# Kernel optimization log

Hardware: AMD Instinct MI355X
Metric: run time of the kernel (lower is better)

Reference implementation:

```python
import jax, jax.numpy as jnp
import numpy as np
from jax import lax

DN = ('NCHW', 'OIHW', 'NCHW')


def conv_s2(x, w, b):
    # Conv2d(kernel=4, stride=2, padding=1): halves H,W
    y = lax.conv_general_dilated(x, w, (2, 2), ((1, 1), (1, 1)), dimension_numbers=DN)
    return y + b[None, :, None, None]


def conv_1x1(x, w, b):
    y = lax.conv_general_dilated(x, w, (1, 1), ((0, 0), (0, 0)), dimension_numbers=DN)
    return y + b[None, :, None, None]


def convT_s2(x, w, b):
    # torch ConvTranspose2d(kernel=4, stride=2, padding=1); torch weight layout [I,O,kh,kw]
    wt = jnp.flip(w, (2, 3)).transpose(1, 0, 2, 3)  # -> [O,I,kh,kw], spatially flipped
    y = lax.conv_general_dilated(x, wt, (1, 1), ((2, 2), (2, 2)),
                                 lhs_dilation=(2, 2), dimension_numbers=DN)
    return y + b[None, :, None, None]


def setup_inputs() -> dict:
    key = jax.random.key(0)
    ks = jax.random.split(key, 20)
    f32 = jnp.float32
    s = 0.05  # small init scale to keep activations sane
    inp = {
        'x': jax.random.uniform(ks[0], (32, 3, 256, 256), dtype=f32),
        # encoder
        'ew1': jax.random.normal(ks[1], (128, 3, 4, 4), f32) * s,
        'eb1': jnp.zeros((128,), f32),
        'ew2': jax.random.normal(ks[2], (256, 128, 4, 4), f32) * s,
        'eb2': jnp.zeros((256,), f32),
        'ew3': jax.random.normal(ks[3], (512, 256, 4, 4), f32) * s,
        'eb3': jnp.zeros((512,), f32),
        # pre-VQ 1x1 conv
        'pw': jax.random.normal(ks[4], (64, 512, 1, 1), f32) * s,
        'pb': jnp.zeros((64,), f32),
        # codebook (torch.randn in module)
        'emb': jax.random.normal(ks[5], (512, 64), f32),
        # decoder (ConvTranspose2d weights: [in, out, kh, kw])
        'dw1': jax.random.normal(ks[6], (64, 256, 4, 4), f32) * s,
        'db1': jnp.zeros((256,), f32),
        'dw2': jax.random.normal(ks[7], (256, 128, 4, 4), f32) * s,
        'db2': jnp.zeros((128,), f32),
        'dw3': jax.random.normal(ks[8], (128, 3, 4, 4), f32) * s,
        'db3': jnp.zeros((3,), f32),
    }
    return inp


def reference(x, ew1, eb1, ew2, eb2, ew3, eb3, pw, pb, emb,
              dw1, db1, dw2, db2, dw3, db3):
    # encoder
    h = jax.nn.relu(conv_s2(x, ew1, eb1))
    h = jax.nn.relu(conv_s2(h, ew2, eb2))
    h = jax.nn.relu(conv_s2(h, ew3, eb3))
    z_e = conv_1x1(h, pw, pb)  # [B, D, H, W]

    b, d, hh, ww = z_e.shape
    x_flat = z_e.reshape(b, d, hh * ww).transpose(0, 2, 1)  # [B, HW, D]
    # squared distances via expansion (same math, no [B,HW,K,D] blowup)
    x2 = jnp.sum(x_flat ** 2, axis=-1, keepdims=True)        # [B, HW, 1]
    e2 = jnp.sum(emb ** 2, axis=-1)                          # [K]
    dist = x2 - 2.0 * jnp.einsum('bnd,kd->bnk', x_flat, emb) + e2[None, None, :]
    indices = jnp.argmin(dist, axis=2)                       # [B, HW]
    zq_flat = emb[indices]                                   # [B, HW, D]
    z_q = zq_flat.transpose(0, 2, 1).reshape(b, d, hh, ww)

    quant_loss = (jnp.mean((zq_flat - x_flat) ** 2) * 2.0)   # matches detach-symmetric mse in fwd value

    # decoder
    y = jax.nn.relu(convT_s2(z_q, dw1, db1))
    y = jax.nn.relu(convT_s2(y, dw2, db2))
    y = jax.nn.sigmoid(convT_s2(y, dw3, db3))
    return (y, quant_loss)
```

## Files before the change

### kernel.cpp

```cpp
#include <hip/hip_runtime.h>
#include <cstddef>

typedef __attribute__((ext_vector_type(8))) _Float16 half8;
typedef __attribute__((ext_vector_type(4))) float f32x4;


template<int CIN>
__global__ __launch_bounds__(256) void wsplit_k(
    const float* __restrict__ W, _Float16* __restrict__ Wh,
    _Float16* __restrict__ Wl, int Cout) {
  constexpr int NCB = CIN / 32;
  int idx = blockIdx.x * 256 + threadIdx.x;
  if (idx >= Cout * CIN) return;
  int ci = idx % CIN, co = idx / CIN;
  int cb = ci >> 5, k8 = (ci >> 3) & 3, j = ci & 7;
  const float* wp = W + (size_t)idx * 16;
#pragma unroll
  for (int tap = 0; tap < 16; ++tap) {
    float w = wp[tap];
    _Float16 wh = (_Float16)w;
    _Float16 wl = (_Float16)((w - (float)wh) * 2048.0f);
    size_t o = (((size_t)(tap * NCB + cb) * 4 + k8) * Cout + co) * 8 + j;
    Wh[o] = wh; Wl[o] = wl;
  }
}

template<int CIN>
__global__ __launch_bounds__(256) void wsplitT_k(
    const float* __restrict__ W, _Float16* __restrict__ Wh,
    _Float16* __restrict__ Wl, int Cout) {
  constexpr int NCB = CIN / 32;
  int idx = blockIdx.x * 256 + threadIdx.x;
  if (idx >= CIN * Cout) return;
  int co = idx % Cout, ci = idx / Cout;
  int cb = ci >> 5, k8 = (ci >> 3) & 3, j = ci & 7;
  const float* wp = W + (size_t)idx * 16;
#pragma unroll
  for (int t = 0; t < 16; ++t) {
    int py = (t >> 3) & 1, px = (t >> 2) & 1, i0 = (t >> 1) & 1, i1 = t & 1;
    int kh = py ? (i0 ? 2 : 0) : (i0 ? 3 : 1);
    int kw = px ? (i1 ? 2 : 0) : (i1 ? 3 : 1);
    float w = wp[kh * 4 + kw];
    _Float16 wh = (_Float16)w;
    _Float16 wl = (_Float16)((w - (float)wh) * 2048.0f);
    size_t o = (((size_t)(t * NCB + cb) * 4 + k8) * Cout + co) * 8 + j;
    Wh[o] = wh; Wl[o] = wl;
  }
}

template<int CIN, int COUT, int CGRP, int RELU>
__global__ __launch_bounds__(256) void conv_mfma2(
    const float* __restrict__ in, const _Float16* __restrict__ Whg,
    const _Float16* __restrict__ Wlg, const float* __restrict__ bias,
    float* __restrict__ out, int Hin, int Win) {
  constexpr int NCB = CIN / 32;
  constexpr int MT  = COUT / CGRP;
  constexpr int MF  = MT / 64;
  const int Hout = Hin >> 1, Wout = Win >> 1;
  const int TW = Wout >> 4;
  __shared__ half8 Bh[4 * 346], Bl[4 * 346];
  const int tid = threadIdx.x;
  const int lane = tid & 63, w = tid >> 6;
  const int l15 = lane & 15, k8 = lane >> 4;
  const int tx = blockIdx.x % TW, ty = blockIdx.x / TW;
  const int cg = blockIdx.y % CGRP;
  const int b  = blockIdx.y / CGRP;
  const int oy0 = ty << 2, ox0 = tx << 4;
  const int iy_org = 2 * oy0 - 1, ix_org = 2 * ox0 - 1;
  const int cbase = cg * MT + w * (MT / 4);
  const float* ip = in + (size_t)b * CIN * Hin * Win;
  const size_t tapStride = (size_t)NCB * 4 * COUT * 8;
  const size_t HW = (size_t)Hin * Win;

  f32x4 accM[MF][4], accX[MF][4];
#pragma unroll
  for (int m = 0; m < MF; ++m)
#pragma unroll
    for (int nf = 0; nf < 4; ++nf) {
      accM[m][nf] = f32x4{0,0,0,0};
      accX[m][nf] = f32x4{0,0,0,0};
    }

  for (int cb = 0; cb < NCB; ++cb) {
    __syncthreads();
    for (int s = tid; s < 340; s += 256) {
      int hy = s / 34, hx = s - hy * 34;
      int iy = iy_org + hy, ix = ix_org + hx;
      bool ok = (unsigned)iy < (unsigned)Hin && (unsigned)ix < (unsigned)Win;
      const float* gp = ip + (size_t)cb * 32 * HW + (ptrdiff_t)iy * Win + ix;
      int slotBase = (hy * 2 + (hx & 1)) * 17 + (hx >> 1);
#pragma unroll
      for (int kk = 0; kk < 4; ++kk) {
        half8 vh, vl;
#pragma unroll
        for (int j = 0; j < 8; ++j) {
          float x = ok ? gp[(size_t)(kk * 8 + j) * HW] : 0.0f;
          _Float16 xh = (_Float16)x;
          vh[j] = xh; vl[j] = (_Float16)((x - (float)xh) * 2048.0f);
        }
        Bh[kk * 346 + slotBase] = vh;
        Bl[kk * 346 + slotBase] = vl;
      }
    }
    __syncthreads();
    const _Float16* aph = Whg + (((size_t)cb * 4 + k8) * COUT + cbase + l15) * 8;
    const _Float16* apl = Wlg + (((size_t)cb * 4 + k8) * COUT + cbase + l15) * 8;
    half8 ah[2][MF], al[2][MF];
#pragma unroll
    for (int m = 0; m < MF; ++m) {
      ah[0][m] = *(const half8*)(aph + m * 128);
      al[0][m] = *(const half8*)(apl + m * 128);
    }
#pragma unroll
    for (int tp = 0; tp < 16; ++tp) {
      const int cur = tp & 1, nxt = cur ^ 1;
      if (tp < 15) {
#pragma unroll
        for (int m = 0; m < MF; ++m) {
          ah[nxt][m] = *(const half8*)(aph + (size_t)(tp + 1) * tapStride + m * 128);
          al[nxt][m] = *(const half8*)(apl + (size_t)(tp + 1) * tapStride + m * 128);
        }
      }
      const int kh = tp >> 2, kw = tp & 3;
      const int p = kw & 1, cidx = kw >> 1;
#pragma unroll
      for (int nf = 0; nf < 4; ++nf) {
        const int slot = k8 * 346 + ((2 * nf + kh) * 2 + p) * 17 + l15 + cidx;
        const half8 bh = Bh[slot], bl = Bl[slot];
#pragma unroll
        for (int m = 0; m < MF; ++m) {
          accM[m][nf] = __builtin_amdgcn_mfma_f32_16x16x32_f16(ah[cur][m], bh, accM[m][nf], 0, 0, 0);
          accX[m][nf] = __builtin_amdgcn_mfma_f32_16x16x32_f16(ah[cur][m], bl, accX[m][nf], 0, 0, 0);
          accX[m][nf] = __builtin_amdgcn_mfma_f32_16x16x32_f16(al[cur][m], bh, accX[m][nf], 0, 0, 0);
        }
      }
    }
  }
#pragma unroll
  for (int m = 0; m < MF; ++m)
#pragma unroll
    for (int nf = 0; nf < 4; ++nf) {
      int oy = oy0 + nf, ox = ox0 + l15;
#pragma unroll
      for (int i = 0; i < 4; ++i) {
        int co = cbase + m * 16 + k8 * 4 + i;
        float v = accM[m][nf][i] + accX[m][nf][i] * (1.0f / 2048.0f) + bias[co];
        if (RELU) v = fmaxf(v, 0.0f);
        out[(((size_t)b * COUT + co) * Hout + oy) * Wout + ox] = v;
      }
    }
}

template<int CIN, int RELU>
__global__ __launch_bounds__(256) void convT_mfma(
    const float* __restrict__ in, const _Float16* __restrict__ Whg,
    const _Float16* __restrict__ Wlg, const float* __restrict__ bias,
    float* __restrict__ out, int Cout, int Hin, int Win) {
  constexpr int NCB = CIN / 32;
  const int Hout = Hin * 2, Wout = Win * 2;
  const int TW = Win >> 4;
  __shared__ half8 Bh[4 * 72], Bl[4 * 72];
  const int tid = threadIdx.x;
  const int lane = tid & 63, w = tid >> 6;
  const int l15 = lane & 15, k8 = lane >> 4;
  const int tx = blockIdx.x % TW, ty = blockIdx.x / TW;
  const int cbo = blockIdx.y % (Cout >> 6);
  const int b   = blockIdx.y / (Cout >> 6);
  const int ty0 = ty << 1, tx0 = tx << 4;
  const int co0 = (cbo << 6) + (w << 4);
  const float* ip = in + (size_t)b * CIN * Hin * Win;
  const size_t HW = (size_t)Hin * Win;
  const size_t tapStride = (size_t)NCB * 4 * Cout * 8;

  f32x4 accM[4][2], accX[4][2];
#pragma unroll
  for (int p = 0; p < 4; ++p)
#pragma unroll
    for (int nf = 0; nf < 2; ++nf) {
      accM[p][nf] = f32x4{0,0,0,0};
      accX[p][nf] = f32x4{0,0,0,0};
    }

  for (int cb = 0; cb < NCB; ++cb) {
    __syncthreads();
    for (int u = tid; u < 288; u += 256) {
      int pos = u % 72, kk = u / 72;
      int r = pos / 18, c = pos - r * 18;
      int iy = ty0 - 1 + r, ix = tx0 - 1 + c;
      bool ok = (unsigned)iy < (unsigned)Hin && (unsigned)ix < (unsigned)Win;
      const float* gp = ip + ((size_t)cb * 32 + kk * 8) * HW + (ptrdiff_t)iy * Win + ix;
      half8 vh, vl;
#pragma unroll
      for (int j = 0; j < 8; ++j) {
        float x = ok ? gp[(size_t)j * HW] : 0.0f;
        _Float16 xh = (_Float16)x;
        vh[j] = xh; vl[j] = (_Float16)((x - (float)xh) * 2048.0f);
      }
      Bh[kk * 72 + pos] = vh;
      Bl[kk * 72 + pos] = vl;
    }
    __syncthreads();
    const _Float16* aph = Whg + (((size_t)cb * 4 + k8) * Cout + co0 + l15) * 8;
    const _Float16* apl = Wlg + (((size_t)cb * 4 + k8) * Cout + co0 + l15) * 8;
    half8 ahA = *(const half8*)(aph);
    half8 alA = *(const half8*)(apl);
#pragma unroll
    for (int t = 0; t < 16; ++t) {
      half8 ahN, alN;
      if (t < 15) {
        ahN = *(const half8*)(aph + (size_t)(t + 1) * tapStride);
        alN = *(const half8*)(apl + (size_t)(t + 1) * tapStride);
      }
      const int py = (t >> 3) & 1, px = (t >> 2) & 1;
      const int i0 = (t >> 1) & 1, i1 = t & 1;
      const int dy = py ? (i0 ? 0 : 1) : (i0 ? -1 : 0);
      const int dx = px ? (i1 ? 0 : 1) : (i1 ? -1 : 0);
      const int p = py * 2 + px;
#pragma unroll
      for (int nf = 0; nf < 2; ++nf) {
        int slot = k8 * 72 + (nf + 1 + dy) * 18 + (l15 + 1 + dx);
        half8 bh = Bh[slot], bl = Bl[slot];
        accM[p][nf] = __builtin_amdgcn_mfma_f32_16x16x32_f16(ahA, bh, accM[p][nf], 0, 0, 0);
        accX[p][nf] = __builtin_amdgcn_mfma_f32_16x16x32_f16(ahA, bl, accX[p][nf], 0, 0, 0);
        accX[p][nf] = __builtin_amdgcn_mfma_f32_16x16x32_f16(alA, bh, accX[p][nf], 0, 0, 0);
      }
      if (t < 15) { ahA = ahN; alA = alN; }
    }
  }
#pragma unroll
  for (int nf = 0; nf < 2; ++nf) {
#pragma unroll
    for (int i = 0; i < 4; ++i) {
      int co = co0 + k8 * 4 + i;
      float bb = bias[co];
#pragma unroll
      for (int py = 0; py < 2; ++py) {
        float v0 = accM[py * 2 + 0][nf][i] + accX[py * 2 + 0][nf][i] * (1.0f / 2048.0f) + bb;
        float v1 = accM[py * 2 + 1][nf][i] + accX[py * 2 + 1][nf][i] * (1.0f / 2048.0f) + bb;
        if (RELU) { v0 = fmaxf(v0, 0.0f); v1 = fmaxf(v1, 0.0f); }
        int oy = 2 * (ty0 + nf) + py, ox = 2 * (tx0 + l15);
        *(float2*)(out + (((size_t)b * Cout + co) * Hout + oy) * Wout + ox) =
            make_float2(v0, v1);
      }
    }
  }
}


template<int CIN, int G, int RELU>
__global__ __launch_bounds__(256) void conv_t(
    const float* __restrict__ in, const float* __restrict__ wt,
    const float* __restrict__ bias, float* __restrict__ out,
    int Cout, int Hin, int Win) {
  const int Hout = Hin >> 1, Wout = Win >> 1;
  const int TW = Wout >> 4;
  __shared__ float tile[34 * 35];
  int tid = threadIdx.x;
  int oxl = tid & 15, oyl = tid >> 4;
  int tyt = blockIdx.x / TW, txt = blockIdx.x - tyt * TW;
  int oy0 = tyt << 4, ox0 = txt << 4;
  int cg = blockIdx.y % (Cout / G);
  int b  = blockIdx.y / (Cout / G);
  int co0 = cg * G;
  const int iy_org = 2 * oy0 - 1, ix_org = 2 * ox0 - 1;
  const float* ip = in + (size_t)b * CIN * Hin * Win;
  float acc[G];
#pragma unroll
  for (int j = 0; j < G; ++j) acc[j] = bias[co0 + j];
  const int lbase = (2 * oyl) * 35 + 2 * oxl;
  for (int ci = 0; ci < CIN; ++ci) {
    const float* ic = ip + (size_t)ci * Hin * Win;
    __syncthreads();
#pragma unroll
    for (int k = 0; k < 5; ++k) {
      int idx = tid + k * 256;
      if (idx < 34 * 34) {
        int r = idx / 34, c = idx - r * 34;
        int iy = iy_org + r, ix = ix_org + c;
        float v = ((unsigned)iy < (unsigned)Hin && (unsigned)ix < (unsigned)Win)
                      ? ic[(size_t)iy * Win + ix] : 0.0f;
        tile[r * 35 + c] = v;
      }
    }
    __syncthreads();
    float xv[16];
#pragma unroll
    for (int kh = 0; kh < 4; ++kh)
#pragma unroll
      for (int kw = 0; kw < 4; ++kw)
        xv[kh * 4 + kw] = tile[lbase + kh * 35 + kw];
    const float* wc = wt + ((size_t)co0 * CIN + ci) * 16;
#pragma unroll
    for (int j = 0; j < G; ++j) {
      const float* wj = wc + (size_t)j * CIN * 16;
#pragma unroll
      for (int t2 = 0; t2 < 16; ++t2) acc[j] = fmaf(xv[t2], wj[t2], acc[j]);
    }
  }
  size_t cs = (size_t)Hout * Wout;
  float* op = out + ((size_t)(b * Cout + co0) * Hout + (oy0 + oyl)) * Wout + ox0 + oxl;
#pragma unroll
  for (int j = 0; j < G; ++j) {
    float v = acc[j];
    if (RELU) v = fmaxf(v, 0.0f);
    op[(size_t)j * cs] = v;
  }
}

template<int CIN, int G>
__global__ __launch_bounds__(256) void conv1x1_k(
    const float* __restrict__ in, const float* __restrict__ wt,
    const float* __restrict__ bias, float* __restrict__ out,
    int Cout, int HW) {
  int hw = blockIdx.x * 256 + threadIdx.x;
  int cg = blockIdx.y % (Cout / G);
  int b  = blockIdx.y / (Cout / G);
  int co0 = cg * G;
  const float* ip = in + (size_t)b * CIN * HW + hw;
  float acc[G];
#pragma unroll
  for (int j = 0; j < G; ++j) acc[j] = bias[co0 + j];
#pragma unroll 4
  for (int ci = 0; ci < CIN; ++ci) {
    float xv = ip[(size_t)ci * HW];
#pragma unroll
    for (int j = 0; j < G; ++j)
      acc[j] = fmaf(xv, wt[(size_t)(co0 + j) * CIN + ci], acc[j]);
  }
  float* op = out + ((size_t)(b * Cout + co0)) * HW + hw;
#pragma unroll
  for (int j = 0; j < G; ++j) op[(size_t)j * HW] = acc[j];
}

__global__ __launch_bounds__(128) void vq_k(
    const float* __restrict__ ze, const float* __restrict__ emb,
    float* __restrict__ zq, float* __restrict__ partial) {
  __shared__ float4 se4[128 * 16];
  __shared__ float red[128];
  int tid = threadIdx.x;
  int gid = blockIdx.x * 128 + tid;
  int b = gid >> 10, n = gid & 1023;
  const float* zp = ze + ((size_t)b << 16) + n;
  float4 v4[16];
#pragma unroll
  for (int d = 0; d < 16; ++d) {
    v4[d].x = zp[(size_t)(4 * d + 0) << 10];
    v4[d].y = zp[(size_t)(4 * d + 1) << 10];
    v4[d].z = zp[(size_t)(4 * d + 2) << 10];
    v4[d].w = zp[(size_t)(4 * d + 3) << 10];
  }
  float best = 1e30f; int bi = 0;
  for (int c = 0; c < 4; ++c) {
    __syncthreads();
    for (int i = tid; i < 2048; i += 128)
      se4[i] = ((const float4*)emb)[(c << 11) + i];
    __syncthreads();
    for (int k = 0; k < 128; ++k) {
      const float4* e = se4 + (k << 4);
      float s = 0.0f;
#pragma unroll
      for (int d = 0; d < 16; ++d) {
        float4 ev = e[d];
        float t0 = v4[d].x - ev.x; s = fmaf(t0, t0, s);
        float t1 = v4[d].y - ev.y; s = fmaf(t1, t1, s);
        float t2 = v4[d].z - ev.z; s = fmaf(t2, t2, s);
        float t3 = v4[d].w - ev.w; s = fmaf(t3, t3, s);
      }
      if (s < best) { best = s; bi = (c << 7) + k; }
    }
  }
  const float4* eb4 = (const float4*)emb + ((size_t)bi << 4);
  float* qp = zq + ((size_t)b << 16) + n;
  float ls = 0.0f;
#pragma unroll
  for (int d = 0; d < 16; ++d) {
    float4 q = eb4[d];
    qp[(size_t)(4 * d + 0) << 10] = q.x;
    qp[(size_t)(4 * d + 1) << 10] = q.y;
    qp[(size_t)(4 * d + 2) << 10] = q.z;
    qp[(size_t)(4 * d + 3) << 10] = q.w;
    float t0 = q.x - v4[d].x; ls = fmaf(t0, t0, ls);
    float t1 = q.y - v4[d].y; ls = fmaf(t1, t1, ls);
    float t2 = q.z - v4[d].z; ls = fmaf(t2, t2, ls);
    float t3 = q.w - v4[d].w; ls = fmaf(t3, t3, ls);
  }
  red[tid] = ls;
  __syncthreads();
  for (int s = 64; s > 0; s >>= 1) {
    if (tid < s) red[tid] += red[tid + s];
    __syncthreads();
  }
  if (tid == 0) partial[blockIdx.x] = red[0];
}

__global__ __launch_bounds__(256) void loss_fin(
    const float* __restrict__ partial, float* __restrict__ out) {
  __shared__ float red[256];
  int t = threadIdx.x;
  red[t] = partial[t];
  __syncthreads();
  for (int s = 128; s > 0; s >>= 1) {
    if (t < s) red[t] += red[t + s];
    __syncthreads();
  }
  if (t == 0) out[0] = red[0] * (2.0f / 2097152.0f);
}

template<int CIN, int G, int ACT>
__global__ __launch_bounds__(256) void convT_t(
    const float* __restrict__ in, const float* __restrict__ wt,
    const float* __restrict__ bias, float* __restrict__ out,
    int Cout, int Hin, int Win) {
  const int Hout = Hin * 2, Wout = Win * 2;
  const int TW = Win >> 4;
  __shared__ float tile[18 * 19];
  int tid = threadIdx.x;
  int txl = tid & 15, tyl = tid >> 4;
  int tyt = blockIdx.x / TW, txt = blockIdx.x - tyt * TW;
  int ty0 = tyt << 4, tx0 = txt << 4;
  int og = blockIdx.y % (Cout / G);
  int b  = blockIdx.y / (Cout / G);
  int o0 = og * G;
  const int iy_org = ty0 - 1, ix_org = tx0 - 1;
  const float* ip = in + (size_t)b * CIN * Hin * Win;
  float a00[G], a01[G], a10[G], a11[G];
#pragma unroll
  for (int j = 0; j < G; ++j) {
    float bb = bias[o0 + j];
    a00[j] = bb; a01[j] = bb; a10[j] = bb; a11[j] = bb;
  }
  const int lb = tyl * 19 + txl;
  for (int i = 0; i < CIN; ++i) {
    const float* ic = ip + (size_t)i * Hin * Win;
    __syncthreads();
#pragma unroll
    for (int k = 0; k < 2; ++k) {
      int idx = tid + k * 256;
      if (idx < 18 * 18) {
        int r = idx / 18, c = idx - r * 18;
        int iy = iy_org + r, ix = ix_org + c;
        float v = ((unsigned)iy < (unsigned)Hin && (unsigned)ix < (unsigned)Win)
                      ? ic[(size_t)iy * Win + ix] : 0.0f;
        tile[r * 19 + c] = v;
      }
    }
    __syncthreads();
    float x00 = tile[lb],          x01 = tile[lb + 1],      x02 = tile[lb + 2];
    float x10 = tile[lb + 19],     x11 = tile[lb + 20],     x12 = tile[lb + 21];
    float x20 = tile[lb + 38],     x21 = tile[lb + 39],     x22 = tile[lb + 40];
    const float* wv = wt + ((size_t)i * Cout + o0) * 16;
#pragma unroll
    for (int j = 0; j < G; ++j) {
      const float* w4 = wv + j * 16;
      a00[j] = fmaf(x11, w4[5],  fmaf(x10, w4[7],  fmaf(x01, w4[13], fmaf(x00, w4[15], a00[j]))));
      a01[j] = fmaf(x12, w4[4],  fmaf(x11, w4[6],  fmaf(x02, w4[12], fmaf(x01, w4[14], a01[j]))));
      a10[j] = fmaf(x21, w4[1],  fmaf(x20, w4[3],  fmaf(x11, w4[9],  fmaf(x10, w4[11], a10[j]))));
      a11[j] = fmaf(x22, w4[0],  fmaf(x21, w4[2],  fmaf(x12, w4[8],  fmaf(x11, w4[10], a11[j]))));
    }
  }
  size_t cs = (size_t)Hout * Wout;
  int ty = ty0 + tyl, tx = tx0 + txl;
  size_t base = ((size_t)(b * Cout + o0) * Hout + 2 * (size_t)ty) * Wout + 2 * tx;
#pragma unroll
  for (int j = 0; j < G; ++j) {
    float v00 = a00[j], v01 = a01[j], v10 = a10[j], v11 = a11[j];
    if (ACT == 1) {
      v00 = fmaxf(v00, 0.0f); v01 = fmaxf(v01, 0.0f);
      v10 = fmaxf(v10, 0.0f); v11 = fmaxf(v11, 0.0f);
    } else if (ACT == 2) {
      v00 = 1.0f / (1.0f + expf(-v00)); v01 = 1.0f / (1.0f + expf(-v01));
      v10 = 1.0f / (1.0f + expf(-v10)); v11 = 1.0f / (1.0f + expf(-v11));
    }
    *(float2*)(out + base + (size_t)j * cs)        = make_float2(v00, v01);
    *(float2*)(out + base + (size_t)j * cs + Wout) = make_float2(v10, v11);
  }
}

extern "C" void kernel_launch(void* const* d_in, const int* in_sizes, int n_in,
                              void* d_out, int out_size, void* d_ws, size_t ws_size,
                              hipStream_t stream) {
  const float* x   = (const float*)d_in[0];
  const float* ew1 = (const float*)d_in[1];
  const float* eb1 = (const float*)d_in[2];
  const float* ew2 = (const float*)d_in[3];
  const float* eb2 = (const float*)d_in[4];
  const float* ew3 = (const float*)d_in[5];
  const float* eb3 = (const float*)d_in[6];
  const float* pw  = (const float*)d_in[7];
  const float* pb  = (const float*)d_in[8];
  const float* emb = (const float*)d_in[9];
  const float* dw1 = (const float*)d_in[10];
  const float* db1 = (const float*)d_in[11];
  const float* dw2 = (const float*)d_in[12];
  const float* db2 = (const float*)d_in[13];
  const float* dw3 = (const float*)d_in[14];
  const float* db3 = (const float*)d_in[15];
  float* out = (float*)d_out;
  char* ws = (char*)d_ws;

  const size_t PER  = 13107200ull;
  const size_t WEXT = 4096ull + 13631488ull;
  int CB = 32;
  while (CB > 1 && (size_t)CB * PER + WEXT > ws_size) CB >>= 1;
  const size_t SA = (size_t)CB * 8388608ull;
  const size_t SB = (size_t)CB * 4194304ull;
  const size_t SC = (size_t)CB * 262144ull;
  float* A    = (float*)(ws);
  float* Bp   = (float*)(ws + SA);
  float* ze   = (float*)(ws + SA + SB);
  float* zq   = (float*)(ws + SA + SB + SC);
  float* part = (float*)(ws + SA + SB + 2 * SC);
  _Float16* wh2  = (_Float16*)(ws + SA + SB + 2 * SC + 4096);
  _Float16* wl2  = wh2 + 524288;
  _Float16* wh3  = wl2 + 524288;
  _Float16* wl3  = wh3 + 2097152;
  _Float16* whT1 = wl3 + 2097152;
  _Float16* wlT1 = whT1 + 262144;
  _Float16* whT2 = wlT1 + 262144;
  _Float16* wlT2 = whT2 + 524288;

  wsplit_k<128><<<128, 256, 0, stream>>>(ew2, wh2, wl2, 256);
  wsplit_k<256><<<512, 256, 0, stream>>>(ew3, wh3, wl3, 512);
  wsplitT_k<64><<<64,  256, 0, stream>>>(dw1, whT1, wlT1, 256);
  wsplitT_k<256><<<128, 256, 0, stream>>>(dw2, whT2, wlT2, 128);

  for (int c0 = 0; c0 < 32; c0 += CB) {
    const float* xc = x + (size_t)c0 * 3 * 65536;
    float* outc = out + (size_t)c0 * 3 * 65536;
    conv_t<3, 16, 1><<<dim3(64, CB * 8), 256, 0, stream>>>(xc, ew1, eb1, A, 128, 256, 256);
    conv_mfma2<128, 256, 1, 1><<<dim3(64, CB),     256, 0, stream>>>(A,  wh2, wl2, eb2, Bp, 128, 128);
    conv_mfma2<256, 512, 2, 1><<<dim3(16, CB * 2), 256, 0, stream>>>(Bp, wh3, wl3, eb3, A,  64,  64);
    conv1x1_k<512, 4><<<dim3(4, CB * 16), 256, 0, stream>>>(A, pw, pb, ze, 64, 1024);
    vq_k<<<CB * 8, 128, 0, stream>>>(ze, emb, zq, part + (size_t)c0 * 8);
    convT_mfma<64,  1><<<dim3(32,  CB * 4), 256, 0, stream>>>(zq, whT1, wlT1, db1, Bp, 256, 32, 32);
    convT_mfma<256, 1><<<dim3(128, CB * 2), 256, 0, stream>>>(Bp, whT2, wlT2, db2, A, 128, 64, 64);
    convT_t<128, 3, 2><<<dim3(64, CB * 1), 256, 0, stream>>>(A, dw3, db3, outc, 3, 128, 128);
  }
  loss_fin<<<1, 256, 0, stream>>>(part, out + (size_t)(out_size - 1));
}
```

Before: 2.573 ms.

## Store intermediate activations as packed hi/lo fp16 in channel-blocked layout

Producer kernels now write activations as packed fp16 hi/lo pairs in a channel-interleaved [B][C/8][H][W][8] layout. Consumer MFMA kernels then read 32 bytes per position with vector loads instead of eight strided scalar loads, and skip the per-element hi/lo split. The strided-read and conversion cost moves into the producers' epilogues. The conv_mfma2 output tile height also drops from four rows to two (NF=2), doubling the block count, which increases halo overhead but improves occupancy and parallelism.

```diff
diff --git a/kernel.cpp b/kernel.cpp
--- a/kernel.cpp
+++ b/kernel.cpp
@@ -3,6 +3,13 @@
 
 typedef __attribute__((ext_vector_type(8))) _Float16 half8;
 typedef __attribute__((ext_vector_type(4))) float f32x4;
+
+static __device__ __forceinline__ unsigned packhl(float v) {
+  _Float16 h = (_Float16)v;
+  _Float16 l = (_Float16)((v - (float)h) * 2048.0f);
+  return (unsigned)__builtin_bit_cast(unsigned short, h) |
+         ((unsigned)__builtin_bit_cast(unsigned short, l) << 16);
+}
 
 
 template<int CIN>
@@ -48,59 +55,64 @@
   }
 }
 
-template<int CIN, int COUT, int CGRP, int RELU>
+template<int CIN, int COUT, int CGRP, int NF, int RELU, int PACKOUT>
 __global__ __launch_bounds__(256) void conv_mfma2(
-    const float* __restrict__ in, const _Float16* __restrict__ Whg,
+    const unsigned* __restrict__ inU, const _Float16* __restrict__ Whg,
     const _Float16* __restrict__ Wlg, const float* __restrict__ bias,
     float* __restrict__ out, int Hin, int Win) {
-  constexpr int NCB = CIN / 32;
-  constexpr int MT  = COUT / CGRP;
-  constexpr int MF  = MT / 64;
+  constexpr int NCB  = CIN / 32;
+  constexpr int MT   = COUT / CGRP;
+  constexpr int MF   = MT / 64;
+  constexpr int ROWS = 2 * NF + 2;
+  constexpr int NPOS = ROWS * 34;
+  constexpr int K8S  = NPOS + 6;
   const int Hout = Hin >> 1, Wout = Win >> 1;
   const int TW = Wout >> 4;
-  __shared__ half8 Bh[4 * 346], Bl[4 * 346];
+  __shared__ half8 Bh[4 * K8S], Bl[4 * K8S];
   const int tid = threadIdx.x;
   const int lane = tid & 63, w = tid >> 6;
   const int l15 = lane & 15, k8 = lane >> 4;
   const int tx = blockIdx.x % TW, ty = blockIdx.x / TW;
   const int cg = blockIdx.y % CGRP;
   const int b  = blockIdx.y / CGRP;
-  const int oy0 = ty << 2, ox0 = tx << 4;
+  const int oy0 = ty * NF, ox0 = tx << 4;
   const int iy_org = 2 * oy0 - 1, ix_org = 2 * ox0 - 1;
   const int cbase = cg * MT + w * (MT / 4);
-  const float* ip = in + (size_t)b * CIN * Hin * Win;
+  const size_t HW = (size_t)Hin * Win;
   const size_t tapStride = (size_t)NCB * 4 * COUT * 8;
-  const size_t HW = (size_t)Hin * Win;
-
-  f32x4 accM[MF][4], accX[MF][4];
+
+  f32x4 accM[MF][NF], accX[MF][NF];
 #pragma unroll
   for (int m = 0; m < MF; ++m)
 #pragma unroll
-    for (int nf = 0; nf < 4; ++nf) {
+    for (int nf = 0; nf < NF; ++nf) {
       accM[m][nf] = f32x4{0,0,0,0};
       accX[m][nf] = f32x4{0,0,0,0};
     }
 
   for (int cb = 0; cb < NCB; ++cb) {
     __syncthreads();
-    for (int s = tid; s < 340; s += 256) {
-      int hy = s / 34, hx = s - hy * 34;
+    for (int u = tid; u < NPOS * 4; u += 256) {
+      int kk = u / NPOS, pos = u - kk * NPOS;
+      int hy = pos / 34, hx = pos - hy * 34;
       int iy = iy_org + hy, ix = ix_org + hx;
       bool ok = (unsigned)iy < (unsigned)Hin && (unsigned)ix < (unsigned)Win;
-      const float* gp = ip + (size_t)cb * 32 * HW + (ptrdiff_t)iy * Win + ix;
+      uint4 qa = {0,0,0,0}, qb = {0,0,0,0};
+      if (ok) {
+        const uint4* gp = (const uint4*)(inU +
+            (((size_t)b * (CIN / 8) + cb * 4 + kk) * HW + (size_t)iy * Win + ix) * 8);
+        qa = gp[0]; qb = gp[1];
+      }
+      unsigned av[8] = {qa.x, qa.y, qa.z, qa.w, qb.x, qb.y, qb.z, qb.w};
+      half8 vh, vl;
+#pragma unroll
+      for (int j = 0; j < 8; ++j) {
+        vh[j] = __builtin_bit_cast(_Float16, (unsigned short)(av[j] & 0xffffu));
+        vl[j] = __builtin_bit_cast(_Float16, (unsigned short)(av[j] >> 16));
+      }
       int slotBase = (hy * 2 + (hx & 1)) * 17 + (hx >> 1);
-#pragma unroll
-      for (int kk = 0; kk < 4; ++kk) {
-        half8 vh, vl;
-#pragma unroll
-        for (int j = 0; j < 8; ++j) {
-          float x = ok ? gp[(size_t)(kk * 8 + j) * HW] : 0.0f;
-          _Float16 xh = (_Float16)x;
-          vh[j] = xh; vl[j] = (_Float16)((x - (float)xh) * 2048.0f);
-        }
-        Bh[kk * 346 + slotBase] = vh;
-        Bl[kk * 346 + slotBase] = vl;
-      }
+      Bh[kk * K8S + slotBase] = vh;
+      Bl[kk * K8S + slotBase] = vl;
     }
     __syncthreads();
     const _Float16* aph = Whg + (((size_t)cb * 4 + k8) * COUT + cbase + l15) * 8;
@@ -124,8 +136,8 @@
       const int kh = tp >> 2, kw = tp & 3;
       const int p = kw & 1, cidx = kw >> 1;
 #pragma unroll
-      for (int nf = 0; nf < 4; ++nf) {
-        const int slot = k8 * 346 + ((2 * nf + kh) * 2 + p) * 17 + l15 + cidx;
+      for (int nf = 0; nf < NF; ++nf) {
+        const int slot = k8 * K8S + ((2 * nf + kh) * 2 + p) * 17 + l15 + cidx;
         const half8 bh = Bh[slot], bl = Bl[slot];
 #pragma unroll
         for (int m = 0; m < MF; ++m) {
@@ -139,19 +151,36 @@
 #pragma unroll
   for (int m = 0; m < MF; ++m)
 #pragma unroll
-    for (int nf = 0; nf < 4; ++nf) {
+    for (int nf = 0; nf < NF; ++nf) {
       int oy = oy0 + nf, ox = ox0 + l15;
-#pragma unroll
-      for (int i = 0; i < 4; ++i) {
-        int co = cbase + m * 16 + k8 * 4 + i;
-        float v = accM[m][nf][i] + accX[m][nf][i] * (1.0f / 2048.0f) + bias[co];
-        if (RELU) v = fmaxf(v, 0.0f);
-        out[(((size_t)b * COUT + co) * Hout + oy) * Wout + ox] = v;
-      }
-    }
-}
-
-template<int CIN, int RELU>
+      if (PACKOUT) {
+        unsigned pk[4];
+#pragma unroll
+        for (int i = 0; i < 4; ++i) {
+          int co = cbase + m * 16 + k8 * 4 + i;
+          float v = accM[m][nf][i] + accX[m][nf][i] * (1.0f / 2048.0f) + bias[co];
+          if (RELU) v = fmaxf(v, 0.0f);
+          pk[i] = packhl(v);
+        }
+        int co8 = (cbase + m * 16 + k8 * 4) >> 3;
+        int j0 = (k8 & 1) * 4;
+        unsigned* outU = (unsigned*)out;
+        *(uint4*)(outU + (((size_t)b * (COUT / 8) + co8) * ((size_t)Hout * Wout)
+                          + (size_t)oy * Wout + ox) * 8 + j0) =
+            make_uint4(pk[0], pk[1], pk[2], pk[3]);
+      } else {
+#pragma unroll
+        for (int i = 0; i < 4; ++i) {
+          int co = cbase + m * 16 + k8 * 4 + i;
+          float v = accM[m][nf][i] + accX[m][nf][i] * (1.0f / 2048.0f) + bias[co];
+          if (RELU) v = fmaxf(v, 0.0f);
+          out[(((size_t)b * COUT + co) * Hout + oy) * Wout + ox] = v;
+        }
+      }
+    }
+}
+
+template<int CIN, int RELU, int PACKIN, int PACKOUT>
 __global__ __launch_bounds__(256) void convT_mfma(
     const float* __restrict__ in, const _Float16* __restrict__ Whg,
     const _Float16* __restrict__ Wlg, const float* __restrict__ bias,
@@ -168,7 +197,6 @@
   const int b   = blockIdx.y / (Cout >> 6);
   const int ty0 = ty << 1, tx0 = tx << 4;
   const int co0 = (cbo << 6) + (w << 4);
-  const float* ip = in + (size_t)b * CIN * Hin * Win;
   const size_t HW = (size_t)Hin * Win;
   const size_t tapStride = (size_t)NCB * 4 * Cout * 8;
 
@@ -188,13 +216,29 @@
       int r = pos / 18, c = pos - r * 18;
       int iy = ty0 - 1 + r, ix = tx0 - 1 + c;
       bool ok = (unsigned)iy < (unsigned)Hin && (unsigned)ix < (unsigned)Win;
-      const float* gp = ip + ((size_t)cb * 32 + kk * 8) * HW + (ptrdiff_t)iy * Win + ix;
       half8 vh, vl;
-#pragma unroll
-      for (int j = 0; j < 8; ++j) {
-        float x = ok ? gp[(size_t)j * HW] : 0.0f;
-        _Float16 xh = (_Float16)x;
-        vh[j] = xh; vl[j] = (_Float16)((x - (float)xh) * 2048.0f);
+      if (PACKIN) {
+        uint4 qa = {0,0,0,0}, qb = {0,0,0,0};
+        if (ok) {
+          const uint4* gp = (const uint4*)((const unsigned*)in +
+              (((size_t)b * (CIN / 8) + cb * 4 + kk) * HW + (size_t)iy * Win + ix) * 8);
+          qa = gp[0]; qb = gp[1];
+        }
+        unsigned av[8] = {qa.x, qa.y, qa.z, qa.w, qb.x, qb.y, qb.z, qb.w};
+#pragma unroll
+        for (int j = 0; j < 8; ++j) {
+          vh[j] = __builtin_bit_cast(_Float16, (unsigned short)(av[j] & 0xffffu));
+          vl[j] = __builtin_bit_cast(_Float16, (unsigned short)(av[j] >> 16));
+        }
+      } else {
+        const float* gp = in + ((size_t)b * CIN + cb * 32 + kk * 8) * HW
+                          + (ptrdiff_t)iy * Win + ix;
+#pragma unroll
+        for (int j = 0; j < 8; ++j) {
+          float x = ok ? gp[(size_t)j * HW] : 0.0f;
+          _Float16 xh = (_Float16)x;
+          vh[j] = xh; vl[j] = (_Float16)((x - (float)xh) * 2048.0f);
+        }
       }
       Bh[kk * 72 + pos] = vh;
       Bl[kk * 72 + pos] = vl;
@@ -239,15 +283,24 @@
         float v1 = accM[py * 2 + 1][nf][i] + accX[py * 2 + 1][nf][i] * (1.0f / 2048.0f) + bb;
         if (RELU) { v0 = fmaxf(v0, 0.0f); v1 = fmaxf(v1, 0.0f); }
         int oy = 2 * (ty0 + nf) + py, ox = 2 * (tx0 + l15);
-        *(float2*)(out + (((size_t)b * Cout + co) * Hout + oy) * Wout + ox) =
-            make_float2(v0, v1);
-      }
-    }
-  }
-}
-
-
-template<int CIN, int G, int RELU>
+        if (PACKOUT) {
+          unsigned* outU = (unsigned*)out;
+          int co8 = (co0 >> 3) + (k8 >> 1);
+          int j = (k8 * 4 + i) & 7;
+          size_t base = ((size_t)b * (Cout / 8) + co8) * ((size_t)Hout * Wout);
+          outU[(base + (size_t)oy * Wout + ox) * 8 + j]     = packhl(v0);
+          outU[(base + (size_t)oy * Wout + ox + 1) * 8 + j] = packhl(v1);
+        } else {
+          *(float2*)(out + (((size_t)b * Cout + co) * Hout + oy) * Wout + ox) =
+              make_float2(v0, v1);
+        }
+      }
+    }
+  }
+}
+
+
+template<int CIN, int G, int RELU, int PACKOUT>
 __global__ __launch_bounds__(256) void conv_t(
     const float* __restrict__ in, const float* __restrict__ wt,
     const float* __restrict__ bias, float* __restrict__ out,
@@ -297,13 +350,29 @@
       for (int t2 = 0; t2 < 16; ++t2) acc[j] = fmaf(xv[t2], wj[t2], acc[j]);
     }
   }
-  size_t cs = (size_t)Hout * Wout;
-  float* op = out + ((size_t)(b * Cout + co0) * Hout + (oy0 + oyl)) * Wout + ox0 + oxl;
-#pragma unroll
-  for (int j = 0; j < G; ++j) {
-    float v = acc[j];
-    if (RELU) v = fmaxf(v, 0.0f);
-    op[(size_t)j * cs] = v;
+  int oy = oy0 + oyl, ox = ox0 + oxl;
+  if (RELU) {
+#pragma unroll
+    for (int j = 0; j < G; ++j) acc[j] = fmaxf(acc[j], 0.0f);
+  }
+  if (PACKOUT) {
+    unsigned* outU = (unsigned*)out;
+    size_t cs = (size_t)Hout * Wout;
+#pragma unroll
+    for (int mb = 0; mb < G / 8; ++mb) {
+      unsigned pk[8];
+#pragma unroll
+      for (int j = 0; j < 8; ++j) pk[j] = packhl(acc[mb * 8 + j]);
+      size_t base = (((size_t)b * (Cout / 8) + (co0 >> 3) + mb) * cs
+                     + (size_t)oy * Wout + ox) * 8;
+      *(uint4*)(outU + base)     = make_uint4(pk[0], pk[1], pk[2], pk[3]);
+      *(uint4*)(outU + base + 4) = make_uint4(pk[4], pk[5], pk[6], pk[7]);
+    }
+  } else {
+    size_t cs = (size_t)Hout * Wout;
+    float* op = out + ((size_t)(b * Cout + co0) * Hout + oy) * Wout + ox;
+#pragma unroll
+    for (int j = 0; j < G; ++j) op[(size_t)j * cs] = acc[j];
   }
 }
 
@@ -527,13 +596,15 @@
   for (int c0 = 0; c0 < 32; c0 += CB) {
     const float* xc = x + (size_t)c0 * 3 * 65536;
     float* outc = out + (size_t)c0 * 3 * 65536;
-    conv_t<3, 16, 1><<<dim3(64, CB * 8), 256, 0, stream>>>(xc, ew1, eb1, A, 128, 256, 256);
-    conv_mfma2<128, 256, 1, 1><<<dim3(64, CB),     256, 0, stream>>>(A,  wh2, wl2, eb2, Bp, 128, 128);
-    conv_mfma2<256, 512, 2, 1><<<dim3(16, CB * 2), 256, 0, stream>>>(Bp, wh3, wl3, eb3, A,  64,  64);
+    conv_t<3, 16, 1, 1><<<dim3(64, CB * 8), 256, 0, stream>>>(xc, ew1, eb1, A, 128, 256, 256);
+    conv_mfma2<128, 256, 1, 2, 1, 1><<<dim3(128, CB),    256, 0, stream>>>(
+        (const unsigned*)A,  wh2, wl2, eb2, Bp, 128, 128);
+    conv_mfma2<256, 512, 2, 2, 1, 0><<<dim3(32, CB * 2), 256, 0, stream>>>(
+        (const unsigned*)Bp, wh3, wl3, eb3, A, 64, 64);
     conv1x1_k<512, 4><<<dim3(4, CB * 16), 256, 0, stream>>>(A, pw, pb, ze, 64, 1024);
     vq_k<<<CB * 8, 128, 0, stream>>>(ze, emb, zq, part + (size_t)c0 * 8);
-    convT_mfma<64,  1><<<dim3(32,  CB * 4), 256, 0, stream>>>(zq, whT1, wlT1, db1, Bp, 256, 32, 32);
-    convT_mfma<256, 1><<<dim3(128, CB * 2), 256, 0, stream>>>(Bp, whT2, wlT2, db2, A, 128, 64, 64);
+    convT_mfma<64,  1, 0, 1><<<dim3(32,  CB * 4), 256, 0, stream>>>(zq, whT1, wlT1, db1, Bp, 256, 32, 32);
+    convT_mfma<256, 1, 1, 0><<<dim3(128, CB * 2), 256, 0, stream>>>(Bp, whT2, wlT2, db2, A, 128, 64, 64);
     convT_t<128, 3, 2><<<dim3(64, CB * 1), 256, 0, stream>>>(A, dw3, db3, outc, 3, 128, 128);
   }
   loss_fin<<<1, 256, 0, stream>>>(part, out + (size_t)(out_size - 1));
```

After: 2.341 ms. 9.0% less time.
